# Performance work log

Measured on AMD Instinct MI355X. Metric: run time of the kernel, lower is better.

## Reference

```python
import jax, jax.numpy as jnp
import numpy as np

PATCH_SIZE = 64
NUM_PATCHES = 32
PRUNE_RATE = 0.1


def setup_inputs() -> dict:
    key = jax.random.key(0)
    k1, k2, k3, k4 = jax.random.split(key, 4)
    B, L, H, E = 8, 1024, 8, 64
    queries = jax.random.normal(k1, (B, L, H, E), dtype=jnp.float32)
    keys = jax.random.normal(k2, (B, L, H, E), dtype=jnp.float32)
    values = jax.random.normal(k3, (B, L, H, E), dtype=jnp.float32)
    # random.randint(0, L - patch_size) is inclusive -> maxval = L - patch_size + 1
    starts = jax.random.randint(k4, (NUM_PATCHES,), 0, L - PATCH_SIZE + 1, dtype=jnp.int32)
    return {"queries": queries, "keys": keys, "values": values, "starts": starts}


def _patch_mask(starts, L):
    # in_patch[p, i] = start_p <= i < start_p + PATCH_SIZE
    idx = jnp.arange(L)
    in_patch = (idx[None, :] >= starts[:, None]) & (idx[None, :] < starts[:, None] + PATCH_SIZE)
    f = in_patch.astype(jnp.float32)
    # union over patches of outer-product block masks -> [L, L]
    return jnp.einsum('pi,pj->ij', f, f) > 0


def reference(queries, keys, values, starts):
    B, L, H, E = queries.shape
    mask = _patch_mask(starts, L)                              # [L, L]
    # dense per-head dot products; zero outside the patch blocks (as torch fills)
    scores = jnp.einsum('blhe,bshe->bhls', queries, keys)      # [B, H, L, L]
    scores = jnp.where(mask[None, None], scores, jnp.float32(0.0))
    abs_scores = jnp.abs(scores)
    # torch.quantile default 'linear' interpolation == jnp.quantile default
    threshold = jnp.quantile(abs_scores, PRUNE_RATE, axis=-1, keepdims=True)
    scores = jnp.where(abs_scores < threshold, -jnp.inf, scores)
    A = jax.nn.softmax(scores, axis=-1)                        # dropout p=0.0 -> identity
    V = jnp.einsum('bhls,bshd->blhd', A, values)               # [B, L, H, D]
    return V
```

## Files before the change

### kernel.cpp

```cpp
#include <hip/hip_runtime.h>

#define LQ 1024
#define HN 8
#define EN 64
#define NP 32
#define NCH 16
#define CC 2.0611536224385579e-9f

typedef __attribute__((ext_vector_type(8))) short short8v;
typedef __attribute__((ext_vector_type(4))) float f32x4;

__device__ __forceinline__ unsigned short bf16hi(float f) {
  unsigned u = __float_as_uint(f);
  u += 0x7fffu + ((u >> 16) & 1u);
  return (unsigned short)(u >> 16);
}
__device__ __forceinline__ float bf16tof(unsigned short b) {
  return __uint_as_float(((unsigned)b) << 16);
}

__global__ __launch_bounds__(512) void sumv_kernel(const float* __restrict__ V,
                                                   float* __restrict__ partial) {
  const int b  = blockIdx.x >> 4;
  const int ch = blockIdx.x & 15;
  const int d  = threadIdx.x;
  const float* Vp = V + (size_t)b * LQ * 512 + (size_t)ch * 64 * 512 + d;
  float p = 0.f;
#pragma unroll 8
  for (int j = 0; j < 64; ++j) p += Vp[(size_t)j * 512];
  partial[(size_t)blockIdx.x * 512 + d] = p;
}

__global__ __launch_bounds__(256) void attn_kernel(const float* __restrict__ Q,
                                                   const float* __restrict__ K,
                                                   const float* __restrict__ V,
                                                   const int* __restrict__ starts,
                                                   const float* __restrict__ partial,
                                                   float* __restrict__ out) {
  __shared__ unsigned short Khi[4096], Klo[4096], Vthi[4096], Plds[4096];
  __shared__ int lotab[64], hitab[64];

  const int tid = threadIdx.x;
  const int l  = tid & 63;
  const int w  = tid >> 6;
  const int lr = l & 15;
  const int lg = l >> 4;
  const int blk = blockIdx.x;
  const int grp = blk & 15, h = (blk >> 4) & 7, b = blk >> 7;
  const int L0 = grp << 6;
  int w0 = grp * 64 - 64;
  w0 = w0 < 0 ? 0 : (w0 > LQ - 192 ? LQ - 192 : w0);

  const float* Qb = Q + (size_t)b * LQ * 512 + h * 64;
  const float* Kb = K + (size_t)b * LQ * 512 + h * 64;
  const float* Vb = V + (size_t)b * LQ * 512 + h * 64;

  if (tid < 64) {
    int row = L0 + tid, lo = 0x7fffffff, hi = 0;
#pragma unroll
    for (int p = 0; p < NP; ++p) {
      int sp = starts[p];
      if ((unsigned)(row - sp) < 64u) { lo = min(lo, sp); hi = max(hi, sp + 64); }
    }
    lotab[tid] = lo; hitab[tid] = hi;
  }

  const float* Qrow = Qb + (size_t)(L0 + w * 16 + lr) * 512;
  short8v qhi[2], qlo[2];
#pragma unroll
  for (int ks = 0; ks < 2; ++ks) {
    float4 a = *(const float4*)(Qrow + ks * 32 + lg * 8);
    float4 c = *(const float4*)(Qrow + ks * 32 + lg * 8 + 4);
    short8v hi8, lo8;
#define CVT8(i, fv) { unsigned short hb_ = bf16hi(fv); hi8[i] = (short)hb_; \
                      lo8[i] = (short)bf16hi((fv) - bf16tof(hb_)); }
    CVT8(0, a.x) CVT8(1, a.y) CVT8(2, a.z) CVT8(3, a.w)
    CVT8(4, c.x) CVT8(5, c.y) CVT8(6, c.z) CVT8(7, c.w)
    qhi[ks] = hi8; qlo[ks] = lo8;
  }

  auto stage = [&](int cs) {
#pragma unroll
    for (int t = 0; t < 4; ++t) {
      const int f  = t * 256 + tid;
      const int sr = f >> 4, c4 = f & 15;
      const float4 kv = *(const float4*)(Kb + (size_t)(cs + sr) * 512 + c4 * 4);
      ushort4 h4, l4;
#define CVTK(i, fv) { unsigned short hb_ = bf16hi(fv); \
                      ((unsigned short*)&h4)[i] = hb_; \
                      ((unsigned short*)&l4)[i] = bf16hi((fv) - bf16tof(hb_)); }
      CVTK(0, kv.x) CVTK(1, kv.y) CVTK(2, kv.z) CVTK(3, kv.w)
      const int kidx = sr * 64 + (((c4 >> 1) ^ (sr & 7)) * 8) + (c4 & 1) * 4;
      *(ushort4*)&Khi[kidx] = h4;
      *(ushort4*)&Klo[kidx] = l4;
      const float4 vv = *(const float4*)(Vb + (size_t)(cs + sr) * 512 + c4 * 4);
#define CVTV(i, fv) { const int d_ = c4 * 4 + i; \
      Vthi[d_ * 64 + (((sr >> 3) ^ (d_ & 7)) * 8) + (sr & 7)] = bf16hi(fv); }
      CVTV(0, vv.x) CVTV(1, vv.y) CVTV(2, vv.z) CVTV(3, vv.w)
    }
  };

  f32x4 oacc[4];
  float zloc[4] = {0.f, 0.f, 0.f, 0.f};
#pragma unroll
  for (int n = 0; n < 4; ++n) oacc[n] = (f32x4){0.f, 0.f, 0.f, 0.f};

  stage(w0);
  __syncthreads();

  int lo_r[4], hi_r[4];
#pragma unroll
  for (int r = 0; r < 4; ++r) {
    lo_r[r] = lotab[w * 16 + lg * 4 + r];
    hi_r[r] = hitab[w * 16 + lg * 4 + r];
  }

  for (int c = 0; c < 3; ++c) {
    const int cs = w0 + c * 64;
    f32x4 sacc[4];
#pragma unroll
    for (int n = 0; n < 4; ++n) sacc[n] = (f32x4){0.f, 0.f, 0.f, 0.f};

#pragma unroll
    for (int ks = 0; ks < 2; ++ks) {
#pragma unroll
      for (int n = 0; n < 4; ++n) {
        const int srow = n * 16 + lr;
        const int idx = srow * 64 + (((ks * 4 + lg) ^ (srow & 7)) * 8);
        const short8v kbh = *(const short8v*)&Khi[idx];
        const short8v kbl = *(const short8v*)&Klo[idx];
        sacc[n] = __builtin_amdgcn_mfma_f32_16x16x32_bf16(qhi[ks], kbh, sacc[n], 0, 0, 0);
        sacc[n] = __builtin_amdgcn_mfma_f32_16x16x32_bf16(qhi[ks], kbl, sacc[n], 0, 0, 0);
        sacc[n] = __builtin_amdgcn_mfma_f32_16x16x32_bf16(qlo[ks], kbh, sacc[n], 0, 0, 0);
      }
    }

#pragma unroll
    for (int n = 0; n < 4; ++n) {
#pragma unroll
      for (int r = 0; r < 4; ++r) {
        const int sg = cs + n * 16 + lr;
        float p = 0.f;
        if (sg >= lo_r[r] && sg < hi_r[r]) p = __expf(sacc[n][r] - 20.f) - CC;
        const unsigned short pb = bf16hi(p);
        zloc[r] += bf16tof(pb);
        const int prow = w * 16 + lg * 4 + r;
        const int sl = n * 16 + lr;
        Plds[prow * 64 + (((sl >> 3) ^ (prow & 7)) * 8) + (sl & 7)] = pb;
      }
    }

#pragma unroll
    for (int ks = 0; ks < 2; ++ks) {
      const int prow = w * 16 + lr;
      const short8v pa = *(const short8v*)&Plds[prow * 64 + (((ks * 4 + lg) ^ (prow & 7)) * 8)];
#pragma unroll
      for (int n = 0; n < 4; ++n) {
        const int d = n * 16 + lr;
        const short8v vbf = *(const short8v*)&Vthi[d * 64 + (((ks * 4 + lg) ^ (d & 7)) * 8)];
        oacc[n] = __builtin_amdgcn_mfma_f32_16x16x32_bf16(pa, vbf, oacc[n], 0, 0, 0);
      }
    }

    if (c < 2) {
      __syncthreads();
      stage(cs + 64);
      __syncthreads();
    }
  }

#pragma unroll
  for (int r = 0; r < 4; ++r) {
#pragma unroll
    for (int off = 1; off < 16; off <<= 1) zloc[r] += __shfl_xor(zloc[r], off, 64);
  }

  float sv[4];
#pragma unroll
  for (int n = 0; n < 4; ++n) {
    float s = 0.f;
    const float* pp = partial + (size_t)b * NCH * 512 + h * 64 + n * 16 + lr;
#pragma unroll
    for (int ch = 0; ch < NCH; ++ch) s += pp[(size_t)ch * 512];
    sv[n] = s;
  }

  float* Ob = out + ((size_t)b * LQ + L0 + w * 16 + lg * 4) * 512 + h * 64;
#pragma unroll
  for (int r = 0; r < 4; ++r) {
    const float invz = 1.f / (zloc[r] + 1024.f * CC);
#pragma unroll
    for (int n = 0; n < 4; ++n)
      Ob[(size_t)r * 512 + n * 16 + lr] = (oacc[n][r] + CC * sv[n]) * invz;
  }
}

extern "C" void kernel_launch(void* const* d_in, const int* in_sizes, int n_in,
                              void* d_out, int out_size, void* d_ws, size_t ws_size,
                              hipStream_t stream) {
  const float* Q      = (const float*)d_in[0];
  const float* K      = (const float*)d_in[1];
  const float* V      = (const float*)d_in[2];
  const int*   starts = (const int*)d_in[3];
  float* out     = (float*)d_out;
  float* partial = (float*)d_ws;

  sumv_kernel<<<128, 512, 0, stream>>>(V, partial);
  attn_kernel<<<1024, 256, 0, stream>>>(Q, K, V, starts, partial, out);
}
```

Baseline: 119.0 us.

## Precompute bf16 K/V planes in prep kernel, async double-buffered LDS loads, skip empty chunks

A new prep kernel converts K into hi/lo bf16 planes and V into a transposed bf16 plane once per key chunk, and fuses the V column sums into the same pass. The attention kernel then pulls these planes into double-buffered LDS through global_load_lds, overlapping the next chunk's load with current compute. It also skips key chunks that no patch touches and remaps block indices for locality. The cost is an extra intermediate buffer write and read in global memory, plus a second kernel doing more work than the old sum kernel.

```diff
diff --git a/kernel.cpp b/kernel.cpp
--- a/kernel.cpp
+++ b/kernel.cpp
@@ -1,10 +1,7 @@
 #include <hip/hip_runtime.h>
 
 #define LQ 1024
-#define HN 8
-#define EN 64
 #define NP 32
-#define NCH 16
 #define CC 2.0611536224385579e-9f
 
 typedef __attribute__((ext_vector_type(8))) short short8v;
@@ -18,42 +15,89 @@
 __device__ __forceinline__ float bf16tof(unsigned short b) {
   return __uint_as_float(((unsigned)b) << 16);
 }
-
-__global__ __launch_bounds__(512) void sumv_kernel(const float* __restrict__ V,
+__device__ __forceinline__ void gload16(const unsigned short* g, unsigned short* l) {
+  __builtin_amdgcn_global_load_lds(
+      (const __attribute__((address_space(1))) unsigned int*)g,
+      (__attribute__((address_space(3))) unsigned int*)l, 16, 0, 0);
+}
+#define SWZD(d) (((d) & 7) ^ ((d) >> 3))
+
+__global__ __launch_bounds__(256) void prep_kernel(const float* __restrict__ K,
+                                                   const float* __restrict__ V,
+                                                   unsigned short* __restrict__ planes,
                                                    float* __restrict__ partial) {
-  const int b  = blockIdx.x >> 4;
-  const int ch = blockIdx.x & 15;
-  const int d  = threadIdx.x;
-  const float* Vp = V + (size_t)b * LQ * 512 + (size_t)ch * 64 * 512 + d;
-  float p = 0.f;
-#pragma unroll 8
-  for (int j = 0; j < 64; ++j) p += Vp[(size_t)j * 512];
-  partial[(size_t)blockIdx.x * 512 + d] = p;
+  __shared__ unsigned short Vt[4096];
+  __shared__ float red[16][64];
+  const int blk = blockIdx.x;
+  const int sc = blk & 15, h = (blk >> 4) & 7, b = blk >> 7;
+  const int tid = threadIdx.x;
+  unsigned short* pb = planes + (size_t)blk * 12288;
+  const float* Kb = K + ((size_t)b * LQ + sc * 64) * 512 + h * 64;
+  const float* Vb = V + ((size_t)b * LQ + sc * 64) * 512 + h * 64;
+  const int c4 = tid & 15;
+  float facc[4] = {0.f, 0.f, 0.f, 0.f};
+#pragma unroll
+  for (int t = 0; t < 4; ++t) {
+    const int sr = t * 16 + (tid >> 4);
+    const float4 kv = *(const float4*)(Kb + (size_t)sr * 512 + c4 * 4);
+    ushort4 h4, l4;
+    {
+      float fv[4] = {kv.x, kv.y, kv.z, kv.w};
+#pragma unroll
+      for (int i = 0; i < 4; ++i) {
+        unsigned short hb = bf16hi(fv[i]);
+        ((unsigned short*)&h4)[i] = hb;
+        ((unsigned short*)&l4)[i] = bf16hi(fv[i] - bf16tof(hb));
+      }
+    }
+    const int kidx = sr * 64 + (((c4 >> 1) ^ (sr & 7)) * 8) + (c4 & 1) * 4;
+    *(ushort4*)&pb[kidx] = h4;
+    *(ushort4*)&pb[4096 + kidx] = l4;
+    const float4 vv = *(const float4*)(Vb + (size_t)sr * 512 + c4 * 4);
+    {
+      float fv[4] = {vv.x, vv.y, vv.z, vv.w};
+#pragma unroll
+      for (int i = 0; i < 4; ++i) {
+        facc[i] += fv[i];
+        const int d = c4 * 4 + i;
+        Vt[d * 64 + (((sr >> 3) ^ SWZD(d)) * 8) + (sr & 7)] = bf16hi(fv[i]);
+      }
+    }
+  }
+#pragma unroll
+  for (int i = 0; i < 4; ++i) red[tid >> 4][c4 * 4 + i] = facc[i];
+  __syncthreads();
+  if (tid < 64) {
+    float s = 0.f;
+#pragma unroll
+    for (int g = 0; g < 16; ++g) s += red[g][tid];
+    partial[(size_t)blk * 64 + tid] = s;
+  }
+#pragma unroll
+  for (int it = 0; it < 2; ++it) {
+    const int idx = (it * 256 + tid) * 8;
+    *(uint4*)&pb[8192 + idx] = *(const uint4*)&Vt[idx];
+  }
 }
 
 __global__ __launch_bounds__(256) void attn_kernel(const float* __restrict__ Q,
-                                                   const float* __restrict__ K,
-                                                   const float* __restrict__ V,
+                                                   const unsigned short* __restrict__ planes,
                                                    const int* __restrict__ starts,
                                                    const float* __restrict__ partial,
                                                    float* __restrict__ out) {
-  __shared__ unsigned short Khi[4096], Klo[4096], Vthi[4096], Plds[4096];
+  __shared__ unsigned short ldsb[2][12288];
+  __shared__ unsigned short Plds[4096];
   __shared__ int lotab[64], hitab[64];
 
   const int tid = threadIdx.x;
-  const int l  = tid & 63;
-  const int w  = tid >> 6;
-  const int lr = l & 15;
-  const int lg = l >> 4;
-  const int blk = blockIdx.x;
-  const int grp = blk & 15, h = (blk >> 4) & 7, b = blk >> 7;
+  const int lane = tid & 63;
+  const int w = tid >> 6;
+  const int lr = lane & 15, lg = lane >> 4;
+  const int blk = ((blockIdx.x & 7) << 7) | (blockIdx.x >> 3);
+  const int grp = blk & 15, bh = blk >> 4;
+  const int h = bh & 7, b = bh >> 3;
   const int L0 = grp << 6;
-  int w0 = grp * 64 - 64;
-  w0 = w0 < 0 ? 0 : (w0 > LQ - 192 ? LQ - 192 : w0);
-
-  const float* Qb = Q + (size_t)b * LQ * 512 + h * 64;
-  const float* Kb = K + (size_t)b * LQ * 512 + h * 64;
-  const float* Vb = V + (size_t)b * LQ * 512 + h * 64;
+  int w0 = L0 - 64; w0 = w0 < 0 ? 0 : (w0 > LQ - 192 ? LQ - 192 : w0);
 
   if (tid < 64) {
     int row = L0 + tid, lo = 0x7fffffff, hi = 0;
@@ -64,48 +108,58 @@
     }
     lotab[tid] = lo; hitab[tid] = hi;
   }
-
-  const float* Qrow = Qb + (size_t)(L0 + w * 16 + lr) * 512;
+  int lo_l = 0x7fffffff, hi_l = 0;
+  {
+    int row = L0 + lane;
+#pragma unroll
+    for (int p = 0; p < NP; ++p) {
+      int sp = starts[p];
+      if ((unsigned)(row - sp) < 64u) { lo_l = min(lo_l, sp); hi_l = max(hi_l, sp + 64); }
+    }
+  }
+  int rlo = lo_l, rhi = hi_l;
+#pragma unroll
+  for (int off = 32; off; off >>= 1) {
+    rlo = min(rlo, __shfl_xor(rlo, off));
+    rhi = max(rhi, __shfl_xor(rhi, off));
+  }
+  rlo = __builtin_amdgcn_readfirstlane(rlo);
+  rhi = __builtin_amdgcn_readfirstlane(rhi);
+
+  int csl[3], ncs = 0;
+#pragma unroll
+  for (int c = 0; c < 3; ++c) {
+    const int cs = w0 + c * 64;
+    if (cs < rhi && cs + 64 > rlo) csl[ncs++] = cs;
+  }
+
+  const unsigned short* gpb = planes + (size_t)bh * 16 * 12288;
+  auto stage = [&](int cs, int buf) {
+    const unsigned short* gp = gpb + (size_t)(cs >> 6) * 12288 + w * 3072 + lane * 8;
+    unsigned short* lp = &ldsb[buf][w * 3072];
+#pragma unroll
+    for (int k = 0; k < 6; ++k) gload16(gp + k * 512, lp + k * 512);
+  };
+
+  if (ncs) stage(csl[0], 0);
+
+  const float* Qrow = Q + ((size_t)b * LQ + L0 + w * 16 + lr) * 512 + h * 64;
   short8v qhi[2], qlo[2];
 #pragma unroll
   for (int ks = 0; ks < 2; ++ks) {
     float4 a = *(const float4*)(Qrow + ks * 32 + lg * 8);
     float4 c = *(const float4*)(Qrow + ks * 32 + lg * 8 + 4);
     short8v hi8, lo8;
-#define CVT8(i, fv) { unsigned short hb_ = bf16hi(fv); hi8[i] = (short)hb_; \
-                      lo8[i] = (short)bf16hi((fv) - bf16tof(hb_)); }
-    CVT8(0, a.x) CVT8(1, a.y) CVT8(2, a.z) CVT8(3, a.w)
-    CVT8(4, c.x) CVT8(5, c.y) CVT8(6, c.z) CVT8(7, c.w)
+    float fv[8] = {a.x, a.y, a.z, a.w, c.x, c.y, c.z, c.w};
+#pragma unroll
+    for (int i = 0; i < 8; ++i) {
+      unsigned short hb = bf16hi(fv[i]);
+      hi8[i] = (short)hb;
+      lo8[i] = (short)bf16hi(fv[i] - bf16tof(hb));
+    }
     qhi[ks] = hi8; qlo[ks] = lo8;
   }
 
-  auto stage = [&](int cs) {
-#pragma unroll
-    for (int t = 0; t < 4; ++t) {
-      const int f  = t * 256 + tid;
-      const int sr = f >> 4, c4 = f & 15;
-      const float4 kv = *(const float4*)(Kb + (size_t)(cs + sr) * 512 + c4 * 4);
-      ushort4 h4, l4;
-#define CVTK(i, fv) { unsigned short hb_ = bf16hi(fv); \
-                      ((unsigned short*)&h4)[i] = hb_; \
-                      ((unsigned short*)&l4)[i] = bf16hi((fv) - bf16tof(hb_)); }
-      CVTK(0, kv.x) CVTK(1, kv.y) CVTK(2, kv.z) CVTK(3, kv.w)
-      const int kidx = sr * 64 + (((c4 >> 1) ^ (sr & 7)) * 8) + (c4 & 1) * 4;
-      *(ushort4*)&Khi[kidx] = h4;
-      *(ushort4*)&Klo[kidx] = l4;
-      const float4 vv = *(const float4*)(Vb + (size_t)(cs + sr) * 512 + c4 * 4);
-#define CVTV(i, fv) { const int d_ = c4 * 4 + i; \
-      Vthi[d_ * 64 + (((sr >> 3) ^ (d_ & 7)) * 8) + (sr & 7)] = bf16hi(fv); }
-      CVTV(0, vv.x) CVTV(1, vv.y) CVTV(2, vv.z) CVTV(3, vv.w)
-    }
-  };
-
-  f32x4 oacc[4];
-  float zloc[4] = {0.f, 0.f, 0.f, 0.f};
-#pragma unroll
-  for (int n = 0; n < 4; ++n) oacc[n] = (f32x4){0.f, 0.f, 0.f, 0.f};
-
-  stage(w0);
   __syncthreads();
 
   int lo_r[4], hi_r[4];
@@ -115,8 +169,18 @@
     hi_r[r] = hitab[w * 16 + lg * 4 + r];
   }
 
-  for (int c = 0; c < 3; ++c) {
-    const int cs = w0 + c * 64;
+  f32x4 oacc[4];
+  float zloc[4] = {0.f, 0.f, 0.f, 0.f};
+#pragma unroll
+  for (int n = 0; n < 4; ++n) oacc[n] = (f32x4){0.f, 0.f, 0.f, 0.f};
+
+  for (int i = 0; i < ncs; ++i) {
+    if (i + 1 < ncs) stage(csl[i + 1], (i + 1) & 1);
+    const unsigned short* Khi_l = &ldsb[i & 1][0];
+    const unsigned short* Klo_l = &ldsb[i & 1][4096];
+    const unsigned short* Vt_l  = &ldsb[i & 1][8192];
+    const int cs = csl[i];
+
     f32x4 sacc[4];
 #pragma unroll
     for (int n = 0; n < 4; ++n) sacc[n] = (f32x4){0.f, 0.f, 0.f, 0.f};
@@ -127,8 +191,8 @@
       for (int n = 0; n < 4; ++n) {
         const int srow = n * 16 + lr;
         const int idx = srow * 64 + (((ks * 4 + lg) ^ (srow & 7)) * 8);
-        const short8v kbh = *(const short8v*)&Khi[idx];
-        const short8v kbl = *(const short8v*)&Klo[idx];
+        const short8v kbh = *(const short8v*)&Khi_l[idx];
+        const short8v kbl = *(const short8v*)&Klo_l[idx];
         sacc[n] = __builtin_amdgcn_mfma_f32_16x16x32_bf16(qhi[ks], kbh, sacc[n], 0, 0, 0);
         sacc[n] = __builtin_amdgcn_mfma_f32_16x16x32_bf16(qhi[ks], kbl, sacc[n], 0, 0, 0);
         sacc[n] = __builtin_amdgcn_mfma_f32_16x16x32_bf16(qlo[ks], kbh, sacc[n], 0, 0, 0);
@@ -142,31 +206,27 @@
         const int sg = cs + n * 16 + lr;
         float p = 0.f;
         if (sg >= lo_r[r] && sg < hi_r[r]) p = __expf(sacc[n][r] - 20.f) - CC;
-        const unsigned short pb = bf16hi(p);
-        zloc[r] += bf16tof(pb);
+        const unsigned short pb16 = bf16hi(p);
+        zloc[r] += bf16tof(pb16);
         const int prow = w * 16 + lg * 4 + r;
         const int sl = n * 16 + lr;
-        Plds[prow * 64 + (((sl >> 3) ^ (prow & 7)) * 8) + (sl & 7)] = pb;
+        Plds[prow * 64 + (((sl >> 3) ^ ((prow & 7) ^ (prow >> 3))) * 8) + (sl & 7)] = pb16;
       }
     }
 
 #pragma unroll
     for (int ks = 0; ks < 2; ++ks) {
       const int prow = w * 16 + lr;
-      const short8v pa = *(const short8v*)&Plds[prow * 64 + (((ks * 4 + lg) ^ (prow & 7)) * 8)];
+      const short8v pa = *(const short8v*)
+          &Plds[prow * 64 + (((ks * 4 + lg) ^ ((prow & 7) ^ (prow >> 3))) * 8)];
 #pragma unroll
       for (int n = 0; n < 4; ++n) {
         const int d = n * 16 + lr;
-        const short8v vbf = *(const short8v*)&Vthi[d * 64 + (((ks * 4 + lg) ^ (d & 7)) * 8)];
-        oacc[n] = __builtin_amdgcn_mfma_f32_16x16x32_bf16(pa, vbf, oacc[n], 0, 0, 0);
-      }
-    }
-
-    if (c < 2) {
-      __syncthreads();
-      stage(cs + 64);
-      __syncthreads();
-    }
+        const short8v vb = *(const short8v*)&Vt_l[d * 64 + (((ks * 4 + lg) ^ SWZD(d)) * 8)];
+        oacc[n] = __builtin_amdgcn_mfma_f32_16x16x32_bf16(pa, vb, oacc[n], 0, 0, 0);
+      }
+    }
+    __syncthreads();
   }
 
 #pragma unroll
@@ -179,9 +239,9 @@
 #pragma unroll
   for (int n = 0; n < 4; ++n) {
     float s = 0.f;
-    const float* pp = partial + (size_t)b * NCH * 512 + h * 64 + n * 16 + lr;
-#pragma unroll
-    for (int ch = 0; ch < NCH; ++ch) s += pp[(size_t)ch * 512];
+#pragma unroll
+    for (int sc2 = 0; sc2 < 16; ++sc2)
+      s += partial[(size_t)bh * 1024 + sc2 * 64 + n * 16 + lr];
     sv[n] = s;
   }
 
@@ -202,9 +262,10 @@
   const float* K      = (const float*)d_in[1];
   const float* V      = (const float*)d_in[2];
   const int*   starts = (const int*)d_in[3];
-  float* out     = (float*)d_out;
-  float* partial = (float*)d_ws;
-
-  sumv_kernel<<<128, 512, 0, stream>>>(V, partial);
-  attn_kernel<<<1024, 256, 0, stream>>>(Q, K, V, starts, partial, out);
-}
+  float* out = (float*)d_out;
+  unsigned short* planes = (unsigned short*)d_ws;
+  float* partial = (float*)((char*)d_ws + 25165824);
+
+  prep_kernel<<<1024, 256, 0, stream>>>(K, V, planes, partial);
+  attn_kernel<<<1024, 256, 0, stream>>>(Q, planes, starts, partial, out);
+}
```

Result: faster. 114.3 us (-3.9%).
